# Kernel optimization log

Hardware: AMD Instinct MI355X
Metric: run time of the kernel (lower is better)

## Reference

```python
import jax, jax.numpy as jnp
import numpy as np

DIM = 1024
HEADS = 16
DIM_HEAD = 64
INNER = HEADS * DIM_HEAD  # 1024
SCALE = DIM_HEAD ** -0.5


def setup_inputs() -> dict:
    key = jax.random.key(0)
    ks = jax.random.split(key, 6)
    b, n = 4, 2048
    x = jax.random.normal(ks[0], (b, n, DIM), dtype=jnp.float32)
    gamma = jnp.ones((DIM,), dtype=jnp.float32)
    # weights stored (in, out); torch Linear computes x @ W.T with W (out, in)
    w_q = jax.random.normal(ks[1], (DIM, INNER), dtype=jnp.float32) * (DIM ** -0.5)
    w_kv = jax.random.normal(ks[2], (DIM, 2 * INNER), dtype=jnp.float32) * (DIM ** -0.5)
    w_out = jax.random.normal(ks[3], (INNER, DIM), dtype=jnp.float32) * (INNER ** -0.5)
    null_kv = jax.random.normal(ks[4], (2, HEADS, 1, DIM_HEAD), dtype=jnp.float32)
    return {"x": x, "gamma": gamma, "w_q": w_q, "w_kv": w_kv, "w_out": w_out, "null_kv": null_kv}


def _layer_norm(x, gamma):
    mu = jnp.mean(x, axis=-1, keepdims=True)
    var = jnp.var(x, axis=-1, keepdims=True)
    return (x - mu) * jax.lax.rsqrt(var + 1e-5) * gamma  # beta == 0


def reference(x, gamma, w_q, w_kv, w_out, null_kv):
    b, n, _ = x.shape
    xn = _layer_norm(x, gamma)
    q = xn @ w_q  # [b, n, inner]
    kv = xn @ w_kv
    k, v = jnp.split(kv, 2, axis=-1)
    q = q * SCALE

    def to_heads(t):
        return t.reshape(b, n, HEADS, DIM_HEAD).transpose(0, 2, 1, 3)  # b h n d

    q, k, v = map(to_heads, (q, k, v))
    nk = jnp.broadcast_to(null_kv[0][None], (b, HEADS, 1, DIM_HEAD))
    nv = jnp.broadcast_to(null_kv[1][None], (b, HEADS, 1, DIM_HEAD))
    k = jnp.concatenate([nk, k], axis=2)  # b h (n+1) d
    v = jnp.concatenate([nv, v], axis=2)
    sim = jnp.einsum('bhid,bhjd->bhij', q, k)
    attn = jax.nn.softmax(sim, axis=-1)
    out = jnp.einsum('bhij,bhjd->bhid', attn, v)
    out = out.transpose(0, 2, 1, 3).reshape(b, n, INNER)
    return out @ w_out
```

## Files before the change

### kernel.cpp

```cpp
#include <hip/hip_runtime.h>

typedef unsigned short ushort_t;
using f32x4  = __attribute__((ext_vector_type(4))) float;
using bf16x8 = __attribute__((ext_vector_type(8))) __bf16;

typedef __attribute__((address_space(1))) const void gvoid_t;
typedef __attribute__((address_space(3))) void svoid_t;

union Frag {
    uint4    u4;
    bf16x8   b;
    ushort_t s[8];
};

__device__ __forceinline__ ushort_t f2bf(float f) {
    union { float f; unsigned u; } a; a.f = f;
    unsigned u = a.u;
    unsigned r = (u + 0x7fffu + ((u >> 16) & 1u)) >> 16;
    return (ushort_t)r;
}
__device__ __forceinline__ float bf2f(ushort_t b) {
    union { unsigned u; float f; } a; a.u = ((unsigned)b) << 16;
    return a.f;
}
__device__ __forceinline__ unsigned pack2bf(float lo, float hi) {
    union { __bf16 h[2]; unsigned u; } p;
    p.h[0] = (__bf16)lo;
    p.h[1] = (__bf16)hi;
    return p.u;
}

__global__ __launch_bounds__(256)
void ln_kernel(const float* __restrict__ x, const float* __restrict__ gamma,
               ushort_t* __restrict__ xn)
{
    const int row = blockIdx.x;
    const int tid = threadIdx.x;
    const float4 v = *reinterpret_cast<const float4*>(x + (size_t)row * 1024 + tid * 4);

    float s = v.x + v.y + v.z + v.w;
    float q = v.x * v.x + v.y * v.y + v.z * v.z + v.w * v.w;
    #pragma unroll
    for (int off = 1; off <= 32; off <<= 1) {
        s += __shfl_xor(s, off);
        q += __shfl_xor(q, off);
    }
    __shared__ float ss[4], sq[4];
    if ((tid & 63) == 0) { ss[tid >> 6] = s; sq[tid >> 6] = q; }
    __syncthreads();
    const float S  = ss[0] + ss[1] + ss[2] + ss[3];
    const float Q  = sq[0] + sq[1] + sq[2] + sq[3];
    const float mu = S * (1.0f / 1024.0f);
    const float var = Q * (1.0f / 1024.0f) - mu * mu;
    const float rstd = rsqrtf(var + 1e-5f);

    const float4 gm = *reinterpret_cast<const float4*>(gamma + tid * 4);
    ushort4 o;
    o.x = f2bf((v.x - mu) * rstd * gm.x);
    o.y = f2bf((v.y - mu) * rstd * gm.y);
    o.z = f2bf((v.z - mu) * rstd * gm.z);
    o.w = f2bf((v.w - mu) * rstd * gm.w);
    *reinterpret_cast<ushort4*>(xn + (size_t)row * 1024 + tid * 4) = o;
}

__global__ __launch_bounds__(256)
void wt_kernel(const float* __restrict__ w, ushort_t* __restrict__ wt, int K, int N)
{
    __shared__ float tile[32][33];
    const int n0 = blockIdx.x * 32, k0 = blockIdx.y * 32;
    const int tx = threadIdx.x, ty = threadIdx.y;
    #pragma unroll
    for (int i = 0; i < 4; ++i) {
        int r = ty + i * 8;
        tile[r][tx] = w[(size_t)(k0 + r) * N + n0 + tx];
    }
    __syncthreads();
    #pragma unroll
    for (int i = 0; i < 4; ++i) {
        int r = ty + i * 8;
        wt[(size_t)(n0 + r) * K + k0 + tx] = f2bf(tile[tx][r]);
    }
}

#define LDK 40

template<int MODE>
__global__ __launch_bounds__(256)
void gemm_kernel(const ushort_t* __restrict__ A, const ushort_t* __restrict__ Bt,
                 ushort_t* __restrict__ o16a, ushort_t* __restrict__ o16b,
                 float* __restrict__ o32)
{
    __shared__ ushort_t ldsA[128 * LDK];
    __shared__ ushort_t ldsB[128 * LDK];

    const int tid = threadIdx.x;
    const int n0 = blockIdx.x * 128, m0 = blockIdx.y * 128;
    const int w = tid >> 6, l = tid & 63, g = l >> 4, c = l & 15;
    const int wm = w >> 1, wn = w & 1;

    const int srow = tid >> 2, skc = tid & 3;
    const ushort_t* ag0 = A  + (size_t)(m0 + srow)      * 1024 + skc * 8;
    const ushort_t* ag1 = A  + (size_t)(m0 + srow + 64) * 1024 + skc * 8;
    const ushort_t* bg0 = Bt + (size_t)(n0 + srow)      * 1024 + skc * 8;
    const ushort_t* bg1 = Bt + (size_t)(n0 + srow + 64) * 1024 + skc * 8;
    const int l0 = srow * LDK + skc * 8;
    const int l1 = (srow + 64) * LDK + skc * 8;

    f32x4 acc[4][4];
    #pragma unroll
    for (int mi = 0; mi < 4; ++mi)
        #pragma unroll
        for (int ni = 0; ni < 4; ++ni)
            acc[mi][ni] = (f32x4){0.f, 0.f, 0.f, 0.f};

    for (int kt = 0; kt < 32; ++kt) {
        const int ko = kt * 32;
        uint4 a0 = *reinterpret_cast<const uint4*>(ag0 + ko);
        uint4 a1 = *reinterpret_cast<const uint4*>(ag1 + ko);
        uint4 b0 = *reinterpret_cast<const uint4*>(bg0 + ko);
        uint4 b1 = *reinterpret_cast<const uint4*>(bg1 + ko);
        __syncthreads();
        *reinterpret_cast<uint4*>(&ldsA[l0]) = a0;
        *reinterpret_cast<uint4*>(&ldsA[l1]) = a1;
        *reinterpret_cast<uint4*>(&ldsB[l0]) = b0;
        *reinterpret_cast<uint4*>(&ldsB[l1]) = b1;
        __syncthreads();

        Frag af[4], bfr[4];
        #pragma unroll
        for (int mi = 0; mi < 4; ++mi)
            af[mi].u4 = *reinterpret_cast<const uint4*>(&ldsA[(wm * 64 + mi * 16 + c) * LDK + g * 8]);
        #pragma unroll
        for (int ni = 0; ni < 4; ++ni)
            bfr[ni].u4 = *reinterpret_cast<const uint4*>(&ldsB[(wn * 64 + ni * 16 + c) * LDK + g * 8]);
        #pragma unroll
        for (int mi = 0; mi < 4; ++mi)
            #pragma unroll
            for (int ni = 0; ni < 4; ++ni)
                acc[mi][ni] = __builtin_amdgcn_mfma_f32_16x16x32_bf16(
                    af[mi].b, bfr[ni].b, acc[mi][ni], 0, 0, 0);
    }

    #pragma unroll
    for (int mi = 0; mi < 4; ++mi) {
        const int mbase = m0 + wm * 64 + mi * 16 + g * 4;
        #pragma unroll
        for (int ni = 0; ni < 4; ++ni) {
            const int n = n0 + wn * 64 + ni * 16 + c;
            if (MODE == 0) {
                const int hh = n >> 6, d = n & 63;
                #pragma unroll
                for (int r = 0; r < 4; ++r) {
                    const int m = mbase + r;
                    const int b = m >> 11, tok = m & 2047;
                    o16a[(((size_t)b * 16 + hh) * 2048 + tok) * 64 + d] =
                        f2bf(acc[mi][ni][r] * 0.125f);
                }
            } else if (MODE == 1) {
                if (n < 1024) {
                    const int hh = n >> 6, d = n & 63;
                    #pragma unroll
                    for (int r = 0; r < 4; ++r) {
                        const int m = mbase + r;
                        const int b = m >> 11, tok = m & 2047;
                        o16a[(((size_t)b * 16 + hh) * 2048 + tok) * 64 + d] =
                            f2bf(acc[mi][ni][r]);
                    }
                } else {
                    const int nn = n - 1024;
                    const int hh = nn >> 6, d = nn & 63;
                    const int b = mbase >> 11, tok0 = mbase & 2047;
                    ushort4 pv;
                    pv.x = f2bf(acc[mi][ni][0]);
                    pv.y = f2bf(acc[mi][ni][1]);
                    pv.z = f2bf(acc[mi][ni][2]);
                    pv.w = f2bf(acc[mi][ni][3]);
                    *reinterpret_cast<ushort4*>(
                        o16b + (((size_t)b * 16 + hh) * 64 + d) * 2048 + tok0) = pv;
                }
            } else {
                #pragma unroll
                for (int r = 0; r < 4; ++r)
                    o32[(size_t)(mbase + r) * 1024 + n] = acc[mi][ni][r];
            }
        }
    }
}

__global__ __launch_bounds__(512)
void attn_kernel(const ushort_t* __restrict__ q, const ushort_t* __restrict__ k,
                 const ushort_t* __restrict__ vt, const float* __restrict__ nkv,
                 ushort_t* __restrict__ out)
{
    __shared__ ushort_t kvs[2][8192];
    __shared__ ushort_t plds[8][16 * 72];

    const int tid = threadIdx.x;
    const int w = tid >> 6, l = tid & 63, g = l >> 4, c = l & 15;
    const int qb = blockIdx.x, bh = blockIdx.y, h = bh & 15;

    const ushort_t* kb = k  + (size_t)bh * 2048 * 64;
    const ushort_t* vb = vt + (size_t)bh * 64 * 2048;

    const int srow = tid >> 3;
    const int ssl  = (tid & 7) ^ (srow & 7);
    const ushort_t* ksrc = kb + srow * 64 + ssl * 8;
    const ushort_t* vsrc = vb + srow * 2048 + ssl * 8;

    const ushort_t* qbase = q + ((size_t)bh * 2048 + qb * 128 + w * 16) * 64;
    Frag aq[2];
    #pragma unroll
    for (int kk = 0; kk < 2; ++kk)
        aq[kk].u4 = *reinterpret_cast<const uint4*>(qbase + c * 64 + kk * 32 + g * 8);

    float snull = 0.f;
    #pragma unroll
    for (int kk = 0; kk < 2; ++kk) {
        const float4 n0 = *reinterpret_cast<const float4*>(nkv + h * 64 + kk * 32 + g * 8);
        const float4 n1 = *reinterpret_cast<const float4*>(nkv + h * 64 + kk * 32 + g * 8 + 4);
        snull += bf2f(aq[kk].s[0]) * n0.x + bf2f(aq[kk].s[1]) * n0.y
               + bf2f(aq[kk].s[2]) * n0.z + bf2f(aq[kk].s[3]) * n0.w;
        snull += bf2f(aq[kk].s[4]) * n1.x + bf2f(aq[kk].s[5]) * n1.y
               + bf2f(aq[kk].s[6]) * n1.z + bf2f(aq[kk].s[7]) * n1.w;
    }
    snull += __shfl_xor(snull, 16);
    snull += __shfl_xor(snull, 32);

    float m_run = snull;
    float l_run = 1.f;

    f32x4 acc[4];
    #pragma unroll
    for (int nf = 0; nf < 4; ++nf) {
        const float nv = nkv[1024 + h * 64 + nf * 16 + c];
        #pragma unroll
        for (int r = 0; r < 4; ++r) acc[nf][r] = nv;
    }

    ushort_t* pw = &plds[w][0];
    const int swz = c & 7;

    __builtin_amdgcn_global_load_lds((gvoid_t*)(ksrc), (svoid_t*)(&kvs[0][tid * 8]), 16, 0, 0);
    __builtin_amdgcn_global_load_lds((gvoid_t*)(vsrc), (svoid_t*)(&kvs[0][4096 + tid * 8]), 16, 0, 0);
    __syncthreads();

    int cur = 0;
    for (int t = 0; t < 32; ++t) {
        if (t < 31) {
            __builtin_amdgcn_global_load_lds((gvoid_t*)(ksrc + (t + 1) * 4096),
                                             (svoid_t*)(&kvs[cur ^ 1][tid * 8]), 16, 0, 0);
            __builtin_amdgcn_global_load_lds((gvoid_t*)(vsrc + (t + 1) * 64),
                                             (svoid_t*)(&kvs[cur ^ 1][4096 + tid * 8]), 16, 0, 0);
        }
        const ushort_t* kbuf = &kvs[cur][0];
        const ushort_t* vbuf = &kvs[cur][4096];

        Frag bk[4][2];
        #pragma unroll
        for (int nt = 0; nt < 4; ++nt)
            #pragma unroll
            for (int kk = 0; kk < 2; ++kk)
                bk[nt][kk].u4 = *reinterpret_cast<const uint4*>(
                    &kbuf[(nt * 16 + c) * 64 + (((kk << 2) | g) ^ swz) * 8]);

        f32x4 st[4];
        #pragma unroll
        for (int nt = 0; nt < 4; ++nt) {
            f32x4 z = (f32x4){0.f, 0.f, 0.f, 0.f};
            st[nt] = __builtin_amdgcn_mfma_f32_16x16x32_bf16(bk[nt][0].b, aq[0].b, z, 0, 0, 0);
            st[nt] = __builtin_amdgcn_mfma_f32_16x16x32_bf16(bk[nt][1].b, aq[1].b, st[nt], 0, 0, 0);
        }

        Frag bv[4][2];
        #pragma unroll
        for (int nf = 0; nf < 4; ++nf)
            #pragma unroll
            for (int k2 = 0; k2 < 2; ++k2)
                bv[nf][k2].u4 = *reinterpret_cast<const uint4*>(
                    &vbuf[(nf * 16 + c) * 64 + (((k2 << 2) | g) ^ swz) * 8]);

        float m01 = fmaxf(fmaxf(st[0][0], st[0][1]), fmaxf(st[0][2], st[0][3]));
        float m23 = fmaxf(fmaxf(st[1][0], st[1][1]), fmaxf(st[1][2], st[1][3]));
        float m45 = fmaxf(fmaxf(st[2][0], st[2][1]), fmaxf(st[2][2], st[2][3]));
        float m67 = fmaxf(fmaxf(st[3][0], st[3][1]), fmaxf(st[3][2], st[3][3]));
        float pm = fmaxf(fmaxf(m01, m23), fmaxf(m45, m67));
        pm = fmaxf(pm, __shfl_xor(pm, 16));
        pm = fmaxf(pm, __shfl_xor(pm, 32));

        if (__any(pm > m_run + 8.f)) {
            const float nm = fmaxf(m_run, pm);
            const float alpha = __expf(m_run - nm);
            m_run = nm;
            l_run *= alpha;
            float av[4];
            #pragma unroll
            for (int r = 0; r < 4; ++r) av[r] = __shfl(alpha, g * 4 + r);
            #pragma unroll
            for (int nf = 0; nf < 4; ++nf)
                #pragma unroll
                for (int r = 0; r < 4; ++r)
                    acc[nf][r] *= av[r];
        }

        #pragma unroll
        for (int nt = 0; nt < 4; ++nt)
            #pragma unroll
            for (int r = 0; r < 4; ++r)
                st[nt][r] = __expf(st[nt][r] - m_run);

        float s0 = (st[0][0] + st[0][1]) + (st[0][2] + st[0][3]);
        float s1 = (st[1][0] + st[1][1]) + (st[1][2] + st[1][3]);
        float s2 = (st[2][0] + st[2][1]) + (st[2][2] + st[2][3]);
        float s3 = (st[3][0] + st[3][1]) + (st[3][2] + st[3][3]);
        float ts = (s0 + s1) + (s2 + s3);
        ts += __shfl_xor(ts, 16);
        ts += __shfl_xor(ts, 32);
        l_run += ts;

        #pragma unroll
        for (int nt = 0; nt < 4; ++nt)
            #pragma unroll
            for (int j = 0; j < 2; ++j)
                *reinterpret_cast<unsigned*>(&pw[c * 72 + nt * 16 + g * 4 + 2 * j]) =
                    pack2bf(st[nt][2 * j], st[nt][2 * j + 1]);

        Frag pa[2];
        #pragma unroll
        for (int k2 = 0; k2 < 2; ++k2)
            pa[k2].u4 = *reinterpret_cast<const uint4*>(&pw[c * 72 + k2 * 32 + g * 8]);

        #pragma unroll
        for (int nf = 0; nf < 4; ++nf) {
            acc[nf] = __builtin_amdgcn_mfma_f32_16x16x32_bf16(pa[0].b, bv[nf][0].b, acc[nf], 0, 0, 0);
            acc[nf] = __builtin_amdgcn_mfma_f32_16x16x32_bf16(pa[1].b, bv[nf][1].b, acc[nf], 0, 0, 0);
        }

        __syncthreads();
        cur ^= 1;
    }

    const size_t ob = ((size_t)(bh >> 4) * 2048 + qb * 128 + w * 16) * 1024 + h * 64;
    #pragma unroll
    for (int r = 0; r < 4; ++r) {
        const float inv = 1.f / __shfl(l_run, g * 4 + r);
        #pragma unroll
        for (int nf = 0; nf < 4; ++nf)
            out[ob + (size_t)(g * 4 + r) * 1024 + nf * 16 + c] = f2bf(acc[nf][r] * inv);
    }
}

extern "C" void kernel_launch(void* const* d_in, const int* in_sizes, int n_in,
                              void* d_out, int out_size, void* d_ws, size_t ws_size,
                              hipStream_t stream)
{
    (void)in_sizes; (void)n_in; (void)out_size; (void)ws_size;
    const float* x     = (const float*)d_in[0];
    const float* gamma = (const float*)d_in[1];
    const float* w_q   = (const float*)d_in[2];
    const float* w_kv  = (const float*)d_in[3];
    const float* w_out = (const float*)d_in[4];
    const float* nkv   = (const float*)d_in[5];
    float* out = (float*)d_out;

    char* ws = (char*)d_ws;
    ushort_t* xn   = (ushort_t*)(ws);
    ushort_t* wqT  = (ushort_t*)(ws + 16777216);
    ushort_t* wkvT = (ushort_t*)(ws + 18874368);
    ushort_t* woT  = (ushort_t*)(ws + 23068672);
    ushort_t* qh   = (ushort_t*)(ws + 25165824);
    ushort_t* kh   = (ushort_t*)(ws + 41943040);
    ushort_t* vtb  = (ushort_t*)(ws + 58720256);
    ushort_t* ao   = xn;

    ln_kernel<<<dim3(8192), dim3(256), 0, stream>>>(x, gamma, xn);
    wt_kernel<<<dim3(32, 32), dim3(32, 8), 0, stream>>>(w_q,  wqT, 1024, 1024);
    wt_kernel<<<dim3(64, 32), dim3(32, 8), 0, stream>>>(w_kv, wkvT, 1024, 2048);
    wt_kernel<<<dim3(32, 32), dim3(32, 8), 0, stream>>>(w_out, woT, 1024, 1024);

    gemm_kernel<0><<<dim3(8, 64),  dim3(256), 0, stream>>>(xn, wqT,  qh, nullptr, nullptr);
    gemm_kernel<1><<<dim3(16, 64), dim3(256), 0, stream>>>(xn, wkvT, kh, vtb, nullptr);

    attn_kernel<<<dim3(16, 64), dim3(512), 0, stream>>>(qh, kh, vtb, nkv, ao);

    gemm_kernel<2><<<dim3(8, 64), dim3(256), 0, stream>>>(ao, woT, nullptr, nullptr, out);
}
```

Baseline: 258.0 us.

## Use direct-to-LDS loads with swizzle in GEMM and tune attention softmax/P staging

The GEMM now loads A and B tiles straight into LDS with global_load_lds, using a 64-wide K tile and an XOR swizzle in place of padded register staging, which halves the number of K iterations and barriers. In attention, the row-sum reduction moves out of the loop: each lane keeps a partial sum and the cross-lane shuffles run once at the end. The P staging buffer is swizzled and written with 64-bit stores, and MFMA sections are wrapped in s_setprio. The GEMM still uses a single LDS buffer with no double buffering, so load latency may stay exposed.

```diff
diff --git a/kernel.cpp b/kernel.cpp
--- a/kernel.cpp
+++ b/kernel.cpp
@@ -82,29 +82,30 @@
     }
 }
 
-#define LDK 40
-
 template<int MODE>
 __global__ __launch_bounds__(256)
 void gemm_kernel(const ushort_t* __restrict__ A, const ushort_t* __restrict__ Bt,
                  ushort_t* __restrict__ o16a, ushort_t* __restrict__ o16b,
                  float* __restrict__ o32)
 {
-    __shared__ ushort_t ldsA[128 * LDK];
-    __shared__ ushort_t ldsB[128 * LDK];
+    __shared__ ushort_t ldsA[128 * 64];
+    __shared__ ushort_t ldsB[128 * 64];
 
     const int tid = threadIdx.x;
     const int n0 = blockIdx.x * 128, m0 = blockIdx.y * 128;
     const int w = tid >> 6, l = tid & 63, g = l >> 4, c = l & 15;
     const int wm = w >> 1, wn = w & 1;
 
-    const int srow = tid >> 2, skc = tid & 3;
-    const ushort_t* ag0 = A  + (size_t)(m0 + srow)      * 1024 + skc * 8;
-    const ushort_t* ag1 = A  + (size_t)(m0 + srow + 64) * 1024 + skc * 8;
-    const ushort_t* bg0 = Bt + (size_t)(n0 + srow)      * 1024 + skc * 8;
-    const ushort_t* bg1 = Bt + (size_t)(n0 + srow + 64) * 1024 + skc * 8;
-    const int l0 = srow * LDK + skc * 8;
-    const int l1 = (srow + 64) * LDK + skc * 8;
+    const ushort_t* asrc[4];
+    const ushort_t* bsrc[4];
+    #pragma unroll
+    for (int j = 0; j < 4; ++j) {
+        const int gidx = j * 256 + tid;
+        const int row = gidx >> 3;
+        const int sl  = (gidx & 7) ^ (row & 7);
+        asrc[j] = A  + (size_t)(m0 + row) * 1024 + sl * 8;
+        bsrc[j] = Bt + (size_t)(n0 + row) * 1024 + sl * 8;
+    }
 
     f32x4 acc[4][4];
     #pragma unroll
@@ -113,32 +114,37 @@
         for (int ni = 0; ni < 4; ++ni)
             acc[mi][ni] = (f32x4){0.f, 0.f, 0.f, 0.f};
 
-    for (int kt = 0; kt < 32; ++kt) {
-        const int ko = kt * 32;
-        uint4 a0 = *reinterpret_cast<const uint4*>(ag0 + ko);
-        uint4 a1 = *reinterpret_cast<const uint4*>(ag1 + ko);
-        uint4 b0 = *reinterpret_cast<const uint4*>(bg0 + ko);
-        uint4 b1 = *reinterpret_cast<const uint4*>(bg1 + ko);
+    const int swz = c & 7;
+
+    for (int kt = 0; kt < 16; ++kt) {
+        if (kt) __syncthreads();
+        #pragma unroll
+        for (int j = 0; j < 4; ++j) {
+            __builtin_amdgcn_global_load_lds((gvoid_t*)(asrc[j] + kt * 64),
+                                             (svoid_t*)(&ldsA[(j * 256 + tid) * 8]), 16, 0, 0);
+            __builtin_amdgcn_global_load_lds((gvoid_t*)(bsrc[j] + kt * 64),
+                                             (svoid_t*)(&ldsB[(j * 256 + tid) * 8]), 16, 0, 0);
+        }
         __syncthreads();
-        *reinterpret_cast<uint4*>(&ldsA[l0]) = a0;
-        *reinterpret_cast<uint4*>(&ldsA[l1]) = a1;
-        *reinterpret_cast<uint4*>(&ldsB[l0]) = b0;
-        *reinterpret_cast<uint4*>(&ldsB[l1]) = b1;
-        __syncthreads();
-
-        Frag af[4], bfr[4];
-        #pragma unroll
-        for (int mi = 0; mi < 4; ++mi)
-            af[mi].u4 = *reinterpret_cast<const uint4*>(&ldsA[(wm * 64 + mi * 16 + c) * LDK + g * 8]);
-        #pragma unroll
-        for (int ni = 0; ni < 4; ++ni)
-            bfr[ni].u4 = *reinterpret_cast<const uint4*>(&ldsB[(wn * 64 + ni * 16 + c) * LDK + g * 8]);
-        #pragma unroll
-        for (int mi = 0; mi < 4; ++mi)
+
+        #pragma unroll
+        for (int kk = 0; kk < 2; ++kk) {
+            Frag af[4], bfr[4];
+            #pragma unroll
+            for (int mi = 0; mi < 4; ++mi)
+                af[mi].u4 = *reinterpret_cast<const uint4*>(
+                    &ldsA[(wm * 64 + mi * 16 + c) * 64 + ((((kk << 2) | g)) ^ swz) * 8]);
             #pragma unroll
             for (int ni = 0; ni < 4; ++ni)
-                acc[mi][ni] = __builtin_amdgcn_mfma_f32_16x16x32_bf16(
-                    af[mi].b, bfr[ni].b, acc[mi][ni], 0, 0, 0);
+                bfr[ni].u4 = *reinterpret_cast<const uint4*>(
+                    &ldsB[(wn * 64 + ni * 16 + c) * 64 + ((((kk << 2) | g)) ^ swz) * 8]);
+            #pragma unroll
+            for (int mi = 0; mi < 4; ++mi)
+                #pragma unroll
+                for (int ni = 0; ni < 4; ++ni)
+                    acc[mi][ni] = __builtin_amdgcn_mfma_f32_16x16x32_bf16(
+                        af[mi].b, bfr[ni].b, acc[mi][ni], 0, 0, 0);
+        }
     }
 
     #pragma unroll
@@ -193,7 +199,7 @@
                  ushort_t* __restrict__ out)
 {
     __shared__ ushort_t kvs[2][8192];
-    __shared__ ushort_t plds[8][16 * 72];
+    __shared__ unsigned plds[8][16 * 32];
 
     const int tid = threadIdx.x;
     const int w = tid >> 6, l = tid & 63, g = l >> 4, c = l & 15;
@@ -226,8 +232,8 @@
     snull += __shfl_xor(snull, 16);
     snull += __shfl_xor(snull, 32);
 
-    float m_run = snull;
-    float l_run = 1.f;
+    float m_run  = snull;
+    float l_part = (l < 16) ? 1.f : 0.f;
 
     f32x4 acc[4];
     #pragma unroll
@@ -237,8 +243,9 @@
         for (int r = 0; r < 4; ++r) acc[nf][r] = nv;
     }
 
-    ushort_t* pw = &plds[w][0];
-    const int swz = c & 7;
+    unsigned* pw = &plds[w][0] + c * 32;
+    const int swz  = c & 7;
+    const int swzP = (c & 7) << 2;
 
     __builtin_amdgcn_global_load_lds((gvoid_t*)(ksrc), (svoid_t*)(&kvs[0][tid * 8]), 16, 0, 0);
     __builtin_amdgcn_global_load_lds((gvoid_t*)(vsrc), (svoid_t*)(&kvs[0][4096 + tid * 8]), 16, 0, 0);
@@ -264,12 +271,14 @@
                     &kbuf[(nt * 16 + c) * 64 + (((kk << 2) | g) ^ swz) * 8]);
 
         f32x4 st[4];
+        __builtin_amdgcn_s_setprio(1);
         #pragma unroll
         for (int nt = 0; nt < 4; ++nt) {
             f32x4 z = (f32x4){0.f, 0.f, 0.f, 0.f};
             st[nt] = __builtin_amdgcn_mfma_f32_16x16x32_bf16(bk[nt][0].b, aq[0].b, z, 0, 0, 0);
             st[nt] = __builtin_amdgcn_mfma_f32_16x16x32_bf16(bk[nt][1].b, aq[1].b, st[nt], 0, 0, 0);
         }
+        __builtin_amdgcn_s_setprio(0);
 
         Frag bv[4][2];
         #pragma unroll
@@ -291,7 +300,7 @@
             const float nm = fmaxf(m_run, pm);
             const float alpha = __expf(m_run - nm);
             m_run = nm;
-            l_run *= alpha;
+            l_part *= alpha;
             float av[4];
             #pragma unroll
             for (int r = 0; r < 4; ++r) av[r] = __shfl(alpha, g * 4 + r);
@@ -312,37 +321,40 @@
         float s1 = (st[1][0] + st[1][1]) + (st[1][2] + st[1][3]);
         float s2 = (st[2][0] + st[2][1]) + (st[2][2] + st[2][3]);
         float s3 = (st[3][0] + st[3][1]) + (st[3][2] + st[3][3]);
-        float ts = (s0 + s1) + (s2 + s3);
-        ts += __shfl_xor(ts, 16);
-        ts += __shfl_xor(ts, 32);
-        l_run += ts;
-
-        #pragma unroll
-        for (int nt = 0; nt < 4; ++nt)
-            #pragma unroll
-            for (int j = 0; j < 2; ++j)
-                *reinterpret_cast<unsigned*>(&pw[c * 72 + nt * 16 + g * 4 + 2 * j]) =
-                    pack2bf(st[nt][2 * j], st[nt][2 * j + 1]);
+        l_part += (s0 + s1) + (s2 + s3);
+
+        #pragma unroll
+        for (int nt = 0; nt < 4; ++nt) {
+            uint2 pr;
+            pr.x = pack2bf(st[nt][0], st[nt][1]);
+            pr.y = pack2bf(st[nt][2], st[nt][3]);
+            *reinterpret_cast<uint2*>(&pw[(nt * 8 + 2 * g) ^ swzP]) = pr;
+        }
 
         Frag pa[2];
         #pragma unroll
         for (int k2 = 0; k2 < 2; ++k2)
-            pa[k2].u4 = *reinterpret_cast<const uint4*>(&pw[c * 72 + k2 * 32 + g * 8]);
-
+            pa[k2].u4 = *reinterpret_cast<const uint4*>(&pw[(k2 * 16 + 4 * g) ^ swzP]);
+
+        __builtin_amdgcn_s_setprio(1);
         #pragma unroll
         for (int nf = 0; nf < 4; ++nf) {
             acc[nf] = __builtin_amdgcn_mfma_f32_16x16x32_bf16(pa[0].b, bv[nf][0].b, acc[nf], 0, 0, 0);
             acc[nf] = __builtin_amdgcn_mfma_f32_16x16x32_bf16(pa[1].b, bv[nf][1].b, acc[nf], 0, 0, 0);
         }
+        __builtin_amdgcn_s_setprio(0);
 
         __syncthreads();
         cur ^= 1;
     }
 
+    l_part += __shfl_xor(l_part, 16);
+    l_part += __shfl_xor(l_part, 32);
+
     const size_t ob = ((size_t)(bh >> 4) * 2048 + qb * 128 + w * 16) * 1024 + h * 64;
     #pragma unroll
     for (int r = 0; r < 4; ++r) {
-        const float inv = 1.f / __shfl(l_run, g * 4 + r);
+        const float inv = 1.f / __shfl(l_part, g * 4 + r);
         #pragma unroll
         for (int nf = 0; nf < 4; ++nf)
             out[ob + (size_t)(g * 4 + r) * 1024 + nf * 16 + c] = f2bf(acc[nf][r] * inv);
```

New measurement: 245.9 us. 4.7% less time.
